# Kernel tuning notes

Hardware: AMD Instinct MI355X
Metric: run time of the kernel (lower is better)

## Reference

```python
import jax, jax.numpy as jnp
import numpy as np

N = 1024          # num_rois == nongt_dim
FEAT = 1024       # feat_dim
EMB = 64          # emb_dim
G = 16            # group == fc_dim
DG = FEAT // G    # dim_group = 64
CLS = 80          # coco classes
EPS_POS = 1e-3
EPS_AFF = 1e-6


def setup_inputs() -> dict:
    key = jax.random.key(0)
    ks = jax.random.split(key, 12)
    # valid boxes: xmin,ymin in [0,500), width/height in [1,101)
    xymin = jax.random.uniform(ks[0], (N, 2), dtype=jnp.float32) * 500.0
    wh = 1.0 + jax.random.uniform(ks[1], (N, 2), dtype=jnp.float32) * 100.0
    bbox = jnp.concatenate([xymin[:, :1], xymin[:, 1:], xymin[:, :1] + wh[:, :1], xymin[:, 1:] + wh[:, 1:]], axis=1)
    roi_feat = jax.random.normal(ks[2], (N, FEAT), dtype=jnp.float32)
    s = lambda d: 1.0 / np.sqrt(d)
    return {
        "bbox": bbox,
        "roi_feat": roi_feat,
        "W_pos": jax.random.normal(ks[3], (EMB, G), dtype=jnp.float32) * s(EMB),
        "b_pos": jnp.zeros((G,), jnp.float32),
        "Wq": jax.random.normal(ks[4], (FEAT, FEAT), dtype=jnp.float32) * s(FEAT),
        "bq": jnp.zeros((FEAT,), jnp.float32),
        "Wk": jax.random.normal(ks[5], (FEAT, FEAT), dtype=jnp.float32) * s(FEAT),
        "bk": jnp.zeros((FEAT,), jnp.float32),
        # grouped 1x1 conv: groups=16, in/group=FEAT=1024, out/group=DG=64 -> [G, DG, FEAT]
        "W_conv": jax.random.normal(ks[6], (G, DG, FEAT), dtype=jnp.float32) * s(FEAT),
        "b_conv": jnp.zeros((FEAT,), jnp.float32),
        "W_ro": jax.random.normal(ks[7], (FEAT, CLS), dtype=jnp.float32) * s(FEAT),
        "b_ro": jnp.zeros((CLS,), jnp.float32),
    }


def _position_matrix(bbox):
    xmin, ymin, xmax, ymax = bbox[:, 0], bbox[:, 1], bbox[:, 2], bbox[:, 3]
    w = xmax - xmin + 1.0
    h = ymax - ymin + 1.0
    cx = 0.5 * (xmin + xmax)
    cy = 0.5 * (ymin + ymax)

    def log_clamped(d):
        d = jnp.where(jnp.abs(d) < EPS_POS, EPS_POS, d)
        return jnp.log(jnp.abs(d))

    dx = log_clamped((cx[:, None] - cx[None, :]) / w[:, None])
    dy = log_clamped((cy[:, None] - cy[None, :]) / h[:, None])
    dw = log_clamped(w[:, None] / w[None, :])
    dh = log_clamped(h[:, None] / h[None, :])
    return jnp.stack([dx, dy, dw, dh], axis=2)  # [N, N, 4]


def _position_embedding(pos_mat, feat_dim=EMB, wave_length=1000.0):
    feat_range = jnp.arange(feat_dim // 8, dtype=jnp.float32)          # 8 freqs
    dim_mat = jnp.power(jnp.float32(wave_length), (8.0 / feat_dim) * feat_range)
    div = pos_mat[..., None] / dim_mat                                  # [N, N, 4, 8]
    emb = jnp.concatenate([jnp.sin(div), jnp.cos(div)], axis=-1)        # [N, N, 4, 16]
    return emb.reshape(pos_mat.shape[0], pos_mat.shape[1], feat_dim)    # [N, N, 64]


def reference(bbox, roi_feat, W_pos, b_pos, Wq, bq, Wk, bk, W_conv, b_conv, W_ro, b_ro):
    n = roi_feat.shape[0]
    pos_emb = _position_embedding(_position_matrix(bbox))               # [N, N, 64]
    aff_w = jax.nn.relu(pos_emb @ W_pos + b_pos)                        # [N, N, G]
    aff_w = jnp.transpose(aff_w, (0, 2, 1))                             # [N, G, N]

    q = (roi_feat @ Wq + bq).reshape(n, G, DG)                          # [N, G, DG]
    k = (roi_feat @ Wk + bk).reshape(n, G, DG)
    aff = jnp.einsum('igd,jgd->igj', q, k) * (1.0 / np.sqrt(DG))        # [N, G, N]

    aff_w = jnp.where(aff_w < EPS_AFF, EPS_AFF, aff_w)
    sm = jax.nn.softmax(jnp.log(aff_w) + aff, axis=2)                   # [N, G, N]

    out_t = jnp.einsum('igj,jd->igd', sm, roi_feat)                     # [N, G, FEAT]
    lin = jnp.einsum('igd,gkd->igk', out_t, W_conv).reshape(n, FEAT) + b_conv
    res = roi_feat + lin                                                # [N, FEAT]
    logits = res.sum(axis=0, keepdims=True) @ W_ro + b_ro               # [1, CLS]
    return jax.nn.sigmoid(logits)
```

## Files before the change

kernel.cpp:

```cpp
#include <hip/hip_runtime.h>
#include <hip/hip_bf16.h>
#include <math.h>

#define NN   1024
#define GG   16
#define DGD  64
#define CLS  80
#define SPLIT 4
#define JT_PER 4

typedef __attribute__((ext_vector_type(8))) short short8;
typedef __attribute__((ext_vector_type(4))) float f32x4;
typedef _Float16 half8 __attribute__((ext_vector_type(8)));

__device__ inline void split2t(float x, ushort& h, ushort& l) {
  uint u = __float_as_uint(x);
  h = (ushort)(u >> 16);
  float r = x - __uint_as_float(u & 0xFFFF0000u);
  l = (ushort)(__float_as_uint(r) >> 16);
}

__device__ inline int wslot(int r, int kc) {
  return ((r >> 4) << 6) + ((kc & 3) << 4) + ((r & 15) ^ ((kc & 3) << 2));
}
__device__ inline int rslot(int f, int lane) {
  return (f << 6) + ((lane >> 4) << 4) + ((lane & 15) ^ ((lane >> 4) << 2));
}

__global__ __launch_bounds__(256) void prep_k(
    const float* __restrict__ roi, ushort* __restrict__ roiH, ushort* __restrict__ roiL,
    const float* __restrict__ Wc,  ushort* __restrict__ WcH,  ushort* __restrict__ WcL,
    const float* __restrict__ Wq,  const float* __restrict__ Wk,
    ushort* __restrict__ WqTH, ushort* __restrict__ WqTL,
    ushort* __restrict__ WkTH, ushort* __restrict__ WkTL)
{
  __shared__ float Tl[64][68];
  const int bid = blockIdx.x;
  const int t = threadIdx.x;

  if (bid < 512) {
    const float* src = bid < 256 ? roi : Wc;
    ushort* H = bid < 256 ? roiH : WcH;
    ushort* L = bid < 256 ? roiL : WcL;
    const int base = ((bid & 255) * 256 + t) * 16;
    float v[16];
    *(float4*)&v[0]  = *(const float4*)&src[base];
    *(float4*)&v[4]  = *(const float4*)&src[base + 4];
    *(float4*)&v[8]  = *(const float4*)&src[base + 8];
    *(float4*)&v[12] = *(const float4*)&src[base + 12];
    ushort hs[16], ls[16];
#pragma unroll
    for (int u = 0; u < 16; ++u) split2t(v[u], hs[u], ls[u]);
    *(uint4*)&H[base]     = *(uint4*)&hs[0];
    *(uint4*)&H[base + 8] = *(uint4*)&hs[8];
    *(uint4*)&L[base]     = *(uint4*)&ls[0];
    *(uint4*)&L[base + 8] = *(uint4*)&ls[8];
  } else {
    const int s = bid - 512;
    const float* W = (s >> 8) ? Wk : Wq;
    ushort* H = (s >> 8) ? WkTH : WqTH;
    ushort* L = (s >> 8) ? WkTL : WqTL;
    const int rb = s & 255;
    const int j0 = (rb & 15) * 64, k0 = (rb >> 4) * 64;
    const int r = t >> 2, c = (t & 3) * 16;
#pragma unroll
    for (int u = 0; u < 4; ++u)
      *(float4*)&Tl[r][c + u * 4] = *(const float4*)&W[(k0 + r) * NN + j0 + c + u * 4];
    __syncthreads();
    ushort hs[16], ls[16];
#pragma unroll
    for (int u = 0; u < 16; ++u) split2t(Tl[c + u][r], hs[u], ls[u]);
    const int ob = (j0 + r) * NN + k0 + c;
    *(uint4*)&H[ob]     = *(uint4*)&hs[0];
    *(uint4*)&H[ob + 8] = *(uint4*)&hs[8];
    *(uint4*)&L[ob]     = *(uint4*)&ls[0];
    *(uint4*)&L[ob + 8] = *(uint4*)&ls[8];
  }
}

__global__ __launch_bounds__(256) void fused_m(
    const float* __restrict__ bbox, const float* __restrict__ Wp,
    const float* __restrict__ bp,
    const ushort* __restrict__ roiH, const ushort* __restrict__ roiL,
    const ushort* __restrict__ WqTH, const ushort* __restrict__ WqTL,
    const ushort* __restrict__ WkTH, const ushort* __restrict__ WkTL,
    const ushort* __restrict__ WcH,  const ushort* __restrict__ WcL,
    const float* __restrict__ bq, const float* __restrict__ bk,
    ushort* __restrict__ qHp, ushort* __restrict__ qLp,
    ushort* __restrict__ kHp, ushort* __restrict__ kLp,
    ushort* __restrict__ rwHp, ushort* __restrict__ rwLp,
    float* __restrict__ paff)
{
  __shared__ short8 sAH[256], sAL[256], sBH[256], sBL[256];
  const int bid = blockIdx.x;
  const int t = threadIdx.x, lane = t & 63, w = t >> 6;

  if (bid % 14 < 6) {
    const int gi = (bid / 14) * 6 + (bid % 14);
    const int crow = (lane >> 4) * 4, ccol = lane & 15;
    const int kc = t & 3, r = t >> 2;
    const int sl0 = wslot(r, kc);
    const int wr = w >> 1, wc = w & 1;

    const ushort *AH_, *AL_, *BH_, *BL_;
    const float* bias;
    ushort *OH_, *OL_;
    int j0;
    if (gi < 512) {
      const int z = gi >> 8, rb = gi & 255;
      const int i0 = (rb >> 4) * 64;
      j0 = (rb & 15) * 64;
      AH_ = roiH + (size_t)i0 * NN;
      AL_ = roiL + (size_t)i0 * NN;
      BH_ = z ? WkTH : WqTH;
      BL_ = z ? WkTL : WqTL;
      bias = z ? bk : bq;
      OH_ = (z ? kHp : qHp) + (size_t)i0 * NN;
      OL_ = (z ? kLp : qLp) + (size_t)i0 * NN;
    } else {
      const int s = gi - 512;
      const int g = s >> 4;
      j0 = (s & 15) * 64;
      AH_ = WcH + (size_t)g * DGD * NN;
      AL_ = WcL + (size_t)g * DGD * NN;
      BH_ = roiH;
      BL_ = roiL;
      bias = nullptr;
      OH_ = rwHp + (size_t)g * DGD * NN;
      OL_ = rwLp + (size_t)g * DGD * NN;
    }

    uint4 vah, val, vbh, vbl;
#define LOADT(kt) { const int ka = (kt) * 32 + (kc << 3); \
    vah = *(const uint4*)&AH_[(size_t)r * NN + ka]; \
    val = *(const uint4*)&AL_[(size_t)r * NN + ka]; \
    vbh = *(const uint4*)&BH_[(size_t)(j0 + r) * NN + ka]; \
    vbl = *(const uint4*)&BL_[(size_t)(j0 + r) * NN + ka]; }

    LOADT(0);
    f32x4 acc[2][2] = {};
    for (int kt = 0; kt < 32; ++kt) {
      __syncthreads();
      *(uint4*)&sAH[sl0] = vah; *(uint4*)&sAL[sl0] = val;
      *(uint4*)&sBH[sl0] = vbh; *(uint4*)&sBL[sl0] = vbl;
      __syncthreads();
      if (kt + 1 < 32) LOADT(kt + 1);
      short8 ah[2], al[2], bh[2], bl[2];
#pragma unroll
      for (int f = 0; f < 2; ++f) {
        ah[f] = sAH[rslot(wr * 2 + f, lane)];
        al[f] = sAL[rslot(wr * 2 + f, lane)];
        bh[f] = sBH[rslot(wc * 2 + f, lane)];
        bl[f] = sBL[rslot(wc * 2 + f, lane)];
      }
#pragma unroll
      for (int fm = 0; fm < 2; ++fm)
#pragma unroll
        for (int fn = 0; fn < 2; ++fn) {
          acc[fm][fn] = __builtin_amdgcn_mfma_f32_16x16x32_bf16(ah[fm], bh[fn], acc[fm][fn], 0, 0, 0);
          acc[fm][fn] = __builtin_amdgcn_mfma_f32_16x16x32_bf16(ah[fm], bl[fn], acc[fm][fn], 0, 0, 0);
          acc[fm][fn] = __builtin_amdgcn_mfma_f32_16x16x32_bf16(al[fm], bh[fn], acc[fm][fn], 0, 0, 0);
        }
    }
#undef LOADT
#pragma unroll
    for (int fm = 0; fm < 2; ++fm) {
      const int row = wr * 32 + fm * 16 + crow;
#pragma unroll
      for (int fn = 0; fn < 2; ++fn) {
        const int col = j0 + wc * 32 + fn * 16 + ccol;
        const float bb = bias ? bias[col] : 0.0f;
#pragma unroll
        for (int e = 0; e < 4; ++e) {
          ushort hh, ll; split2t(acc[fm][fn][e] + bb, hh, ll);
          OH_[(size_t)(row + e) * NN + col] = hh;
          OL_[(size_t)(row + e) * NN + col] = ll;
        }
      }
    }
  } else {
    const int i = (bid / 14) * 8 + (bid % 14) - 6;
    half8* sWH = (half8*)sAH;
    half8* sWL = (half8*)sAL;
    float* bpS = (float*)sBH;

    if (t < 128) {
      const int h = t >> 6, kc2 = (t >> 4) & 3, g = t & 15;
      _Float16 hh[8], ll[8];
#pragma unroll
      for (int u = 0; u < 8; ++u) {
        float x = Wp[(h * 32 + kc2 * 8 + u) * 16 + g];
        _Float16 xh = (_Float16)x;
        hh[u] = xh;
        ll[u] = (_Float16)(x - (float)xh);
      }
      sWH[t] = *(half8*)&hh[0];
      sWL[t] = *(half8*)&ll[0];
    }
    if (t < 16) bpS[t] = bp[t];
    __syncthreads();

    const half8 wh0 = sWH[lane], wh1 = sWH[64 + lane];
    const half8 wl0 = sWL[lane], wl1 = sWL[64 + lane];
    const float bb = bpS[lane & 15];

    const float xi0 = bbox[i*4+0], yi0 = bbox[i*4+1], xi1 = bbox[i*4+2], yi1 = bbox[i*4+3];
    const float wi = xi1 - xi0 + 1.0f, hi = yi1 - yi0 + 1.0f;
    const float cxi = 0.5f*(xi0+xi1), cyi = 0.5f*(yi0+yi1);

    const int jr = lane & 15, p = lane >> 4;
    const int csel = p >> 1;
    const bool iscos = (p & 1);
    const float shift = iscos ? 1.5707963267948966f : 0.0f;

    const float invdim[8] = {1.0f, 0.42169650342858224f, 0.17782794100389228f,
        0.07498942093324558f, 0.03162277660168379f, 0.01333521432163324f,
        0.005623413251903491f, 0.0023713737056616554f};

#pragma unroll 1
    for (int f = 0; f < 16; ++f) {
      const int j0 = w * 256 + f * 16;
      float4 bj = *(const float4*)&bbox[(j0 + jr) * 4];
      const float wj = bj.z - bj.x + 1.0f, hj = bj.w - bj.y + 1.0f;
      const float cxj = 0.5f*(bj.x+bj.z), cyj = 0.5f*(bj.y+bj.w);

      const float num1 = csel ? (cyi - cyj) : (cxi - cxj);
      const float den1 = csel ? hi : wi;
      const float pos1 = __logf(fmaxf(fabsf(num1 / den1), 1e-3f));
      const float num2 = csel ? hi : wi;
      const float den2 = csel ? hj : wj;
      const float pos2 = __logf(fmaxf(fabsf(num2 / den2), 1e-3f));

      _Float16 a1[8], a2[8];
#pragma unroll
      for (int u = 0; u < 4; ++u) {
        a1[u] = (_Float16)__sinf(fmaf(pos1, invdim[u], shift));
        a2[u] = (_Float16)__sinf(fmaf(pos2, invdim[u], shift));
      }
#pragma unroll
      for (int u = 4; u < 8; ++u) {
        const float b1 = pos1 * invdim[u];
        const float b2 = pos2 * invdim[u];
        const float q1 = b1 * b1, q2 = b2 * b2;
        const float s1 = b1 * fmaf(q1, -0.16666667f, 1.0f);
        const float c1 = fmaf(q1, -0.5f, 1.0f);
        const float s2 = b2 * fmaf(q2, -0.16666667f, 1.0f);
        const float c2 = fmaf(q2, -0.5f, 1.0f);
        a1[u] = (_Float16)(iscos ? c1 : s1);
        a2[u] = (_Float16)(iscos ? c2 : s2);
      }
      const half8 A1 = *(half8*)&a1[0];
      const half8 A2 = *(half8*)&a2[0];

      f32x4 acc = {0.f, 0.f, 0.f, 0.f};
      acc = __builtin_amdgcn_mfma_f32_16x16x32_f16(A1, wh0, acc, 0, 0, 0);
      acc = __builtin_amdgcn_mfma_f32_16x16x32_f16(A2, wh1, acc, 0, 0, 0);
      acc = __builtin_amdgcn_mfma_f32_16x16x32_f16(A1, wl0, acc, 0, 0, 0);
      acc = __builtin_amdgcn_mfma_f32_16x16x32_f16(A2, wl1, acc, 0, 0, 0);

      float4 ov;
      ov.x = __logf(fmaxf(acc[0] + bb, 1e-6f));
      ov.y = __logf(fmaxf(acc[1] + bb, 1e-6f));
      ov.z = __logf(fmaxf(acc[2] + bb, 1e-6f));
      ov.w = __logf(fmaxf(acc[3] + bb, 1e-6f));
      *(float4*)&paff[((i * GG + (lane & 15)) << 10) + j0 + p * 4] = ov;
    }
  }
}

__global__ __launch_bounds__(256) void attn_m(
    const ushort* __restrict__ qhp, const ushort* __restrict__ qlp,
    const ushort* __restrict__ khp, const ushort* __restrict__ klp,
    const ushort* __restrict__ rwhp, const ushort* __restrict__ rwlp,
    const float* __restrict__ paff,
    float* __restrict__ po, float* __restrict__ pstat)
{
  const int g  = blockIdx.y;
  const int i0 = blockIdx.x * 64;
  const int sp = blockIdx.z;
  const int t  = threadIdx.x;
  const int lane = t & 63, w = t >> 6;

  __shared__ short8 sKH[512], sKL[512], sRH[512], sRL[512];
  __shared__ float PT[4][16][68];

  const int r  = t >> 2;
  const int kc = t & 3;
  const int sl = wslot(r, kc);

  {
    const ushort* s0 = qhp + (size_t)(i0 + r) * NN + g * DGD + kc * 8;
    const ushort* s1 = qlp + (size_t)(i0 + r) * NN + g * DGD + kc * 8;
    *(uint4*)&sKH[sl]       = *(const uint4*)&s0[0];
    *(uint4*)&sKH[sl + 256] = *(const uint4*)&s0[32];
    *(uint4*)&sKL[sl]       = *(const uint4*)&s1[0];
    *(uint4*)&sKL[sl + 256] = *(const uint4*)&s1[32];
  }
  __syncthreads();
  const int qsl = rslot(w, lane);
  const short8 qf_h0 = sKH[qsl], qf_h1 = sKH[256 + qsl];
  const short8 qf_l0 = sKL[qsl], qf_l1 = sKL[256 + qsl];

  const int qr = (lane >> 4) * 4;
  const int qc = lane & 15;

  float m[4], l[4];
  f32x4 o[4] = {};
#pragma unroll
  for (int e = 0; e < 4; ++e) { m[e] = -1e30f; l[e] = 0.f; }

#pragma unroll 1
  for (int jt = sp * JT_PER; jt < sp * JT_PER + JT_PER; ++jt) {
    const int j0 = jt * 64;
    const ushort* ks0 = khp + (size_t)(j0 + r) * NN + g * DGD + kc * 8;
    const ushort* ks1 = klp + (size_t)(j0 + r) * NN + g * DGD + kc * 8;
    uint4 kv00 = *(const uint4*)&ks0[0], kv01 = *(const uint4*)&ks0[32];
    uint4 kv10 = *(const uint4*)&ks1[0], kv11 = *(const uint4*)&ks1[32];
    const ushort* rs0 = rwhp + ((size_t)g * DGD + r) * NN + j0 + kc * 8;
    const ushort* rs1 = rwlp + ((size_t)g * DGD + r) * NN + j0 + kc * 8;
    uint4 rv00 = *(const uint4*)&rs0[0], rv01 = *(const uint4*)&rs0[32];
    uint4 rv10 = *(const uint4*)&rs1[0], rv11 = *(const uint4*)&rs1[32];
    float pf[4][4];
#pragma unroll
    for (int jf = 0; jf < 4; ++jf)
#pragma unroll
      for (int e = 0; e < 4; ++e)
        pf[jf][e] = paff[(((i0 + w * 16 + qr + e) * GG + g) << 10) + j0 + jf * 16 + qc];

    __syncthreads();
    *(uint4*)&sKH[sl] = kv00; *(uint4*)&sKH[sl + 256] = kv01;
    *(uint4*)&sKL[sl] = kv10; *(uint4*)&sKL[sl + 256] = kv11;
    *(uint4*)&sRH[sl] = rv00; *(uint4*)&sRH[sl + 256] = rv01;
    *(uint4*)&sRL[sl] = rv10; *(uint4*)&sRL[sl + 256] = rv11;
    __syncthreads();

    f32x4 s4[4];
#pragma unroll
    for (int jf = 0; jf < 4; ++jf) {
      const int bs = rslot(jf, lane);
      short8 bh0 = sKH[bs], bh1 = sKH[256 + bs];
      short8 bl0 = sKL[bs], bl1 = sKL[256 + bs];
      f32x4 a = {0.f, 0.f, 0.f, 0.f};
      a = __builtin_amdgcn_mfma_f32_16x16x32_bf16(qf_h0, bh0, a, 0, 0, 0);
      a = __builtin_amdgcn_mfma_f32_16x16x32_bf16(qf_h1, bh1, a, 0, 0, 0);
      a = __builtin_amdgcn_mfma_f32_16x16x32_bf16(qf_h0, bl0, a, 0, 0, 0);
      a = __builtin_amdgcn_mfma_f32_16x16x32_bf16(qf_h1, bl1, a, 0, 0, 0);
      a = __builtin_amdgcn_mfma_f32_16x16x32_bf16(qf_l0, bh0, a, 0, 0, 0);
      a = __builtin_amdgcn_mfma_f32_16x16x32_bf16(qf_l1, bh1, a, 0, 0, 0);
      s4[jf] = a;
    }

#pragma unroll
    for (int e = 0; e < 4; ++e) {
      float v0 = fmaf(s4[0][e], 0.125f, pf[0][e]);
      float v1 = fmaf(s4[1][e], 0.125f, pf[1][e]);
      float v2 = fmaf(s4[2][e], 0.125f, pf[2][e]);
      float v3 = fmaf(s4[3][e], 0.125f, pf[3][e]);
      float tm = fmaxf(fmaxf(v0, v1), fmaxf(v2, v3));
#pragma unroll
      for (int off = 1; off < 16; off <<= 1) tm = fmaxf(tm, __shfl_xor(tm, off, 64));
      const float mn = fmaxf(m[e], tm);
      const float sc = __expf(m[e] - mn);
      v0 = __expf(v0 - mn); v1 = __expf(v1 - mn);
      v2 = __expf(v2 - mn); v3 = __expf(v3 - mn);
      float ts = (v0 + v1) + (v2 + v3);
#pragma unroll
      for (int off = 1; off < 16; off <<= 1) ts += __shfl_xor(ts, off, 64);
      l[e] = l[e] * sc + ts;
      m[e] = mn;
#pragma unroll
      for (int nf = 0; nf < 4; ++nf) o[nf][e] *= sc;
      PT[w][qr + e][ 0 + qc] = v0;
      PT[w][qr + e][16 + qc] = v1;
      PT[w][qr + e][32 + qc] = v2;
      PT[w][qr + e][48 + qc] = v3;
    }

    short8 ph[2], pl[2];
#pragma unroll
    for (int h = 0; h < 2; ++h) {
      const float* psrc = &PT[w][lane & 15][h * 32 + (lane >> 4) * 8];
      float4 x = *(const float4*)&psrc[0];
      float4 y = *(const float4*)&psrc[4];
      float vv[8] = {x.x, x.y, x.z, x.w, y.x, y.y, y.z, y.w};
      ushort hh[8], ll[8];
#pragma unroll
      for (int u = 0; u < 8; ++u) split2t(vv[u], hh[u], ll[u]);
      ph[h] = *(short8*)&hh[0];
      pl[h] = *(short8*)&ll[0];
    }

#pragma unroll
    for (int nf = 0; nf < 4; ++nf) {
      const int bs = rslot(nf, lane);
      short8 rh0 = sRH[bs], rh1 = sRH[256 + bs];
      short8 rl0 = sRL[bs], rl1 = sRL[256 + bs];
      f32x4 a = o[nf];
      a = __builtin_amdgcn_mfma_f32_16x16x32_bf16(ph[0], rh0, a, 0, 0, 0);
      a = __builtin_amdgcn_mfma_f32_16x16x32_bf16(ph[1], rh1, a, 0, 0, 0);
      a = __builtin_amdgcn_mfma_f32_16x16x32_bf16(ph[0], rl0, a, 0, 0, 0);
      a = __builtin_amdgcn_mfma_f32_16x16x32_bf16(ph[1], rl1, a, 0, 0, 0);
      a = __builtin_amdgcn_mfma_f32_16x16x32_bf16(pl[0], rh0, a, 0, 0, 0);
      a = __builtin_amdgcn_mfma_f32_16x16x32_bf16(pl[1], rh1, a, 0, 0, 0);
      o[nf] = a;
    }
  }

  const size_t idx = ((size_t)blockIdx.x * GG + g) * SPLIT + sp;
  float* pot = po + idx * 4096;
#pragma unroll
  for (int nf = 0; nf < 4; ++nf)
#pragma unroll
    for (int e = 0; e < 4; ++e)
      pot[(w * 16 + qr + e) * 64 + nf * 16 + qc] = o[nf][e];
  if (qc == 0) {
#pragma unroll
    for (int e = 0; e < 4; ++e) {
      const int row = w * 16 + qr + e;
      pstat[(idx * 64 + row) * 2]     = m[e];
      pstat[(idx * 64 + row) * 2 + 1] = l[e];
    }
  }
}

__global__ __launch_bounds__(256) void combine_k(
    const float* __restrict__ po, const float* __restrict__ pstat,
    const float* __restrict__ roi, const float* __restrict__ bconv,
    float* __restrict__ res)
{
  const int it = blockIdx.x, g = blockIdx.y;
  const int t = threadIdx.x;
  const int row = t >> 2, c0 = (t & 3) * 16;
  const size_t base = ((size_t)it * GG + g) * SPLIT;

  float ms[SPLIT], ls[SPLIT];
#pragma unroll
  for (int s = 0; s < SPLIT; ++s) {
    float2 st = *(const float2*)&pstat[((base + s) * 64 + row) * 2];
    ms[s] = st.x; ls[s] = st.y;
  }
  float M = ms[0];
#pragma unroll
  for (int s = 1; s < SPLIT; ++s) M = fmaxf(M, ms[s]);
  float wgt[SPLIT], L = 0.f;
#pragma unroll
  for (int s = 0; s < SPLIT; ++s) { wgt[s] = __expf(ms[s] - M); L = fmaf(ls[s], wgt[s], L); }
  const float rL = 1.0f / L;

  const int grow = it * 64 + row;
  const int f0   = g * DGD + c0;
#pragma unroll
  for (int c = 0; c < 4; ++c) {
    float4 acc = {0.f, 0.f, 0.f, 0.f};
#pragma unroll
    for (int s = 0; s < SPLIT; ++s) {
      float4 v = *(const float4*)&po[(base + s) * 4096 + row * 64 + c0 + c * 4];
      acc.x = fmaf(v.x, wgt[s], acc.x);
      acc.y = fmaf(v.y, wgt[s], acc.y);
      acc.z = fmaf(v.z, wgt[s], acc.z);
      acc.w = fmaf(v.w, wgt[s], acc.w);
    }
    float4 r4 = *(const float4*)&roi[grow * NN + f0 + c * 4];
    float4 b4 = *(const float4*)&bconv[f0 + c * 4];
    float4 ov;
    ov.x = r4.x + b4.x + acc.x * rL;
    ov.y = r4.y + b4.y + acc.y * rL;
    ov.z = r4.z + b4.z + acc.z * rL;
    ov.w = r4.w + b4.w + acc.w * rL;
    *(float4*)&res[grow * NN + f0 + c * 4] = ov;
  }
}

__global__ __launch_bounds__(256) void colsum_partial_k(
    const float* __restrict__ res, float* __restrict__ part)
{
  const int d  = blockIdx.x * 256 + threadIdx.x;
  const int r0 = blockIdx.y * 128;
  float s0 = 0.f, s1 = 0.f, s2 = 0.f, s3 = 0.f;
  for (int i = 0; i < 128; i += 4) {
    s0 += res[(r0 + i    ) * NN + d];
    s1 += res[(r0 + i + 1) * NN + d];
    s2 += res[(r0 + i + 2) * NN + d];
    s3 += res[(r0 + i + 3) * NN + d];
  }
  part[blockIdx.y * NN + d] = (s0 + s1) + (s2 + s3);
}

__global__ __launch_bounds__(640) void final_k(
    const float* __restrict__ part, const float* __restrict__ W_ro,
    const float* __restrict__ b_ro, float* __restrict__ out)
{
  __shared__ float cs[1024];
  __shared__ float red[8][CLS];
  const int t = threadIdx.x;

  for (int u = t; u < 1024; u += 640) {
    float s = 0.f;
#pragma unroll
    for (int p = 0; p < 8; ++p) s += part[p * NN + u];
    cs[u] = s;
  }
  __syncthreads();

  {
    const int c = t % CLS, s = t / CLS;
    float acc = 0.f;
    const int d0 = s * 128;
#pragma unroll 8
    for (int d = d0; d < d0 + 128; ++d)
      acc = fmaf(cs[d], W_ro[d * CLS + c], acc);
    red[s][c] = acc;
  }
  __syncthreads();

  if (t < CLS) {
    float lg = b_ro[t];
#pragma unroll
    for (int s = 0; s < 8; ++s) lg += red[s][t];
    out[t] = 1.0f / (1.0f + __expf(-lg));
  }
}

extern "C" void kernel_launch(void* const* d_in, const int* in_sizes, int n_in,
                              void* d_out, int out_size, void* d_ws, size_t ws_size,
                              hipStream_t stream) {
  const float* bbox  = (const float*)d_in[0];
  const float* roi   = (const float*)d_in[1];
  const float* W_pos = (const float*)d_in[2];
  const float* b_pos = (const float*)d_in[3];
  const float* Wq    = (const float*)d_in[4];
  const float* bq    = (const float*)d_in[5];
  const float* Wk    = (const float*)d_in[6];
  const float* bk    = (const float*)d_in[7];
  const float* Wc    = (const float*)d_in[8];
  const float* bcv   = (const float*)d_in[9];
  const float* W_ro  = (const float*)d_in[10];
  const float* b_ro  = (const float*)d_in[11];

  float* ws = (float*)d_ws;
  float* paff = ws;
  ushort* roiH = (ushort*)(ws + (16 << 20));
  ushort* roiL = (ushort*)(ws + (16 << 20) + (1 << 19));
  ushort* WqTH = (ushort*)(ws + (17 << 20));
  ushort* WqTL = (ushort*)(ws + (17 << 20) + (1 << 19));
  ushort* WkTH = (ushort*)(ws + (18 << 20));
  ushort* WkTL = (ushort*)(ws + (18 << 20) + (1 << 19));
  ushort* WcH  = (ushort*)(ws + (19 << 20));
  ushort* WcL  = (ushort*)(ws + (19 << 20) + (1 << 19));
  ushort* qHp  = (ushort*)(ws + (20 << 20));
  ushort* qLp  = (ushort*)(ws + (20 << 20) + (1 << 19));
  ushort* kHp  = (ushort*)(ws + (21 << 20));
  ushort* kLp  = (ushort*)(ws + (21 << 20) + (1 << 19));
  ushort* rwHp = (ushort*)(ws + (22 << 20));
  ushort* rwLp = (ushort*)(ws + (22 << 20) + (1 << 19));
  float* po    = ws + (16 << 20);
  float* pstat = ws + (23 << 20);
  float* part  = ws + (23 << 20) + (1 << 18);
  float* res   = ws + (23 << 20) + (1 << 19);

  prep_k<<<1024, 256, 0, stream>>>(roi, roiH, roiL, Wc, WcH, WcL,
                                   Wq, Wk, WqTH, WqTL, WkTH, WkTL);

  fused_m<<<1792, 256, 0, stream>>>(bbox, W_pos, b_pos,
                                    roiH, roiL, WqTH, WqTL, WkTH, WkTL,
                                    WcH, WcL, bq, bk,
                                    qHp, qLp, kHp, kLp, rwHp, rwLp, paff);

  attn_m<<<dim3(16, 16, SPLIT), 256, 0, stream>>>(qHp, qLp, kHp, kLp, rwHp, rwLp,
                                                  paff, po, pstat);
  combine_k<<<dim3(16, 16), 256, 0, stream>>>(po, pstat, roi, bcv, res);
  colsum_partial_k<<<dim3(4, 8), 256, 0, stream>>>(res, part);
  final_k<<<1, 640, 0, stream>>>(part, W_ro, b_ro, (float*)d_out);
}
```

Before: 113.9 us.

## Store log position affinity in fp16 and double attention split-K parallelism

```diff
diff --git a/kernel.cpp b/kernel.cpp
--- a/kernel.cpp
+++ b/kernel.cpp
@@ -6,8 +6,8 @@
 #define GG   16
 #define DGD  64
 #define CLS  80
-#define SPLIT 4
-#define JT_PER 4
+#define SPLIT 8
+#define JT_PER 2
 
 typedef __attribute__((ext_vector_type(8))) short short8;
 typedef __attribute__((ext_vector_type(4))) float f32x4;
@@ -18,6 +18,15 @@
   h = (ushort)(u >> 16);
   float r = x - __uint_as_float(u & 0xFFFF0000u);
   l = (ushort)(__float_as_uint(r) >> 16);
+}
+
+__device__ inline ushort f32tof16(float x) {
+  _Float16 h = (_Float16)x;
+  return *(ushort*)&h;
+}
+__device__ inline float f16tof32(ushort u) {
+  _Float16 h; *(ushort*)&h = u;
+  return (float)h;
 }
 
 __device__ inline int wslot(int r, int kc) {
@@ -89,7 +98,7 @@
     ushort* __restrict__ qHp, ushort* __restrict__ qLp,
     ushort* __restrict__ kHp, ushort* __restrict__ kLp,
     ushort* __restrict__ rwHp, ushort* __restrict__ rwLp,
-    float* __restrict__ paff)
+    ushort* __restrict__ paffh)
 {
   __shared__ short8 sAH[256], sAL[256], sBH[256], sBL[256];
   const int bid = blockIdx.x;
@@ -258,12 +267,12 @@
       acc = __builtin_amdgcn_mfma_f32_16x16x32_f16(A1, wl0, acc, 0, 0, 0);
       acc = __builtin_amdgcn_mfma_f32_16x16x32_f16(A2, wl1, acc, 0, 0, 0);
 
-      float4 ov;
-      ov.x = __logf(fmaxf(acc[0] + bb, 1e-6f));
-      ov.y = __logf(fmaxf(acc[1] + bb, 1e-6f));
-      ov.z = __logf(fmaxf(acc[2] + bb, 1e-6f));
-      ov.w = __logf(fmaxf(acc[3] + bb, 1e-6f));
-      *(float4*)&paff[((i * GG + (lane & 15)) << 10) + j0 + p * 4] = ov;
+      ushort o4[4];
+      o4[0] = f32tof16(__logf(fmaxf(acc[0] + bb, 1e-6f)));
+      o4[1] = f32tof16(__logf(fmaxf(acc[1] + bb, 1e-6f)));
+      o4[2] = f32tof16(__logf(fmaxf(acc[2] + bb, 1e-6f)));
+      o4[3] = f32tof16(__logf(fmaxf(acc[3] + bb, 1e-6f)));
+      *(short4*)&paffh[((i * GG + (lane & 15)) << 10) + j0 + p * 4] = *(short4*)&o4[0];
     }
   }
 }
@@ -272,7 +281,7 @@
     const ushort* __restrict__ qhp, const ushort* __restrict__ qlp,
     const ushort* __restrict__ khp, const ushort* __restrict__ klp,
     const ushort* __restrict__ rwhp, const ushort* __restrict__ rwlp,
-    const float* __restrict__ paff,
+    const ushort* __restrict__ paffh,
     float* __restrict__ po, float* __restrict__ pstat)
 {
   const int g  = blockIdx.y;
@@ -325,7 +334,7 @@
     for (int jf = 0; jf < 4; ++jf)
 #pragma unroll
       for (int e = 0; e < 4; ++e)
-        pf[jf][e] = paff[(((i0 + w * 16 + qr + e) * GG + g) << 10) + j0 + jf * 16 + qc];
+        pf[jf][e] = f16tof32(paffh[(((i0 + w * 16 + qr + e) * GG + g) << 10) + j0 + jf * 16 + qc]);
 
     __syncthreads();
     *(uint4*)&sKH[sl] = kv00; *(uint4*)&sKH[sl + 256] = kv01;
@@ -538,7 +547,8 @@
   const float* b_ro  = (const float*)d_in[11];
 
   float* ws = (float*)d_ws;
-  float* paff = ws;
+  ushort* paffh = (ushort*)ws;
+  float* po = ws + (8 << 20);
   ushort* roiH = (ushort*)(ws + (16 << 20));
   ushort* roiL = (ushort*)(ws + (16 << 20) + (1 << 19));
   ushort* WqTH = (ushort*)(ws + (17 << 20));
@@ -553,7 +563,6 @@
   ushort* kLp  = (ushort*)(ws + (21 << 20) + (1 << 19));
   ushort* rwHp = (ushort*)(ws + (22 << 20));
   ushort* rwLp = (ushort*)(ws + (22 << 20) + (1 << 19));
-  float* po    = ws + (16 << 20);
   float* pstat = ws + (23 << 20);
   float* part  = ws + (23 << 20) + (1 << 18);
   float* res   = ws + (23 << 20) + (1 << 19);
@@ -564,10 +573,10 @@
   fused_m<<<1792, 256, 0, stream>>>(bbox, W_pos, b_pos,
                                     roiH, roiL, WqTH, WqTL, WkTH, WkTL,
                                     WcH, WcL, bq, bk,
-                                    qHp, qLp, kHp, kLp, rwHp, rwLp, paff);
+                                    qHp, qLp, kHp, kLp, rwHp, rwLp, paffh);
 
   attn_m<<<dim3(16, 16, SPLIT), 256, 0, stream>>>(qHp, qLp, kHp, kLp, rwHp, rwLp,
-                                                  paff, po, pstat);
+                                                  paffh, po, pstat);
   combine_k<<<dim3(16, 16), 256, 0, stream>>>(po, pstat, roi, bcv, res);
   colsum_partial_k<<<dim3(4, 8), 256, 0, stream>>>(res, part);
   final_k<<<1, 640, 0, stream>>>(part, W_ro, b_ro, (float*)d_out);
```

After: 121.0 us. +6.3%, slower.
